# Performance work log

Measured on AMD Instinct MI355X. Metric: run time of the kernel, lower is better.

## Reference

```python
import jax, jax.numpy as jnp
import numpy as np

B, S, DIM = 64, 256, 512
H = 16
DH = DIM // H          # 32
W = 256                # window_size == seq_len
ROPE_BASE = 10000.0


def _rope(x):
    # x: (B, S, H, DH), interleaved-pair RoPE
    pos = jnp.arange(S, dtype=jnp.float32)
    inv_freq = 1.0 / (ROPE_BASE ** (jnp.arange(0, DH, 2, dtype=jnp.float32) / DH))
    sinusoid = pos[:, None] * inv_freq[None, :]            # (S, DH/2)
    sin = jnp.sin(sinusoid)[None, :, None, :]              # (1, S, 1, DH/2)
    cos = jnp.cos(sinusoid)[None, :, None, :]
    x1 = x[..., 0::2]
    x2 = x[..., 1::2]
    r1 = x1 * cos - x2 * sin
    r2 = x1 * sin + x2 * cos
    return jnp.stack([r1, r2], axis=-1).reshape(x.shape)


def setup_inputs() -> dict:
    key = jax.random.key(0)
    ks = jax.random.split(key, 8)
    s = 1.0 / np.sqrt(DIM)
    return {
        "hidden_states": jax.random.normal(ks[0], (B, S, DIM), jnp.float32),
        "Wq": jax.random.normal(ks[1], (DIM, DIM), jnp.float32) * s,
        "bq": jnp.zeros((DIM,), jnp.float32),
        "Wk": jax.random.normal(ks[2], (DIM, DIM), jnp.float32) * s,
        "bk": jnp.zeros((DIM,), jnp.float32),
        "Wv": jax.random.normal(ks[3], (DIM, DIM), jnp.float32) * s,
        "bv": jnp.zeros((DIM,), jnp.float32),
        "bias_table": jax.random.normal(ks[4], (2 * W - 1, H), jnp.float32) * 0.02,
    }


def reference(hidden_states, Wq, bq, Wk, bk, Wv, bv, bias_table):
    b, s, _ = hidden_states.shape
    q = hidden_states @ Wq + bq
    k = hidden_states @ Wk + bk
    v = hidden_states @ Wv + bv
    # (B, S, H, DH)
    q = _rope(q.reshape(b, s, H, DH))
    k = _rope(k.reshape(b, s, H, DH))
    v = v.reshape(b, s, H, DH)
    # (B, H, S, DH)
    q = q.transpose(0, 2, 1, 3)
    k = k.transpose(0, 2, 1, 3)
    v = v.transpose(0, 2, 1, 3)
    scores = jnp.einsum('bhqd,bhkd->bhqk', q, k) / np.sqrt(DH)
    # relative_position_index[i, j] == (i - j) + W - 1
    rel_idx = jnp.arange(W)[:, None] - jnp.arange(W)[None, :] + (W - 1)
    rel_bias = bias_table[rel_idx]                 # (W, W, H)
    rel_bias = rel_bias.transpose(2, 0, 1)[None]   # (1, H, W, W)
    # NOTE: bias added AFTER softmax, faithful to the original module
    probs = jax.nn.softmax(scores, axis=-1) + rel_bias
    ctx = jnp.einsum('bhqk,bhkd->bhqd', probs, v)
    ctx = ctx.transpose(0, 2, 1, 3).reshape(b, s, DIM)
    return ctx
```

## Files before the change

kernel.cpp:

```cpp
#include <hip/hip_runtime.h>
#include <stdint.h>

typedef __attribute__((ext_vector_type(8))) short bf16x8;
typedef __attribute__((ext_vector_type(4))) float f32x4;
typedef __attribute__((ext_vector_type(4))) unsigned int u32x4;

#define MFMA16(a, b, c) __builtin_amdgcn_mfma_f32_16x16x32_bf16(a, b, c, 0, 0, 0)

__device__ __forceinline__ float bf2f(unsigned short u) {
    union { unsigned int i; float f; } x; x.i = ((unsigned int)u) << 16; return x.f;
}
__device__ __forceinline__ unsigned short f2bf(float f) {
    union { float f; unsigned int i; } x; x.f = f;
    unsigned int u = x.i;
    return (unsigned short)((u + 0x7FFFu + ((u >> 16) & 1u)) >> 16);
}

__global__ __launch_bounds__(256) void k_cvt(const float4* __restrict__ in,
                                             unsigned short* __restrict__ At) {
    __shared__ unsigned short t[16 * 512];
    const int tid = threadIdx.x;
    const int blk = blockIdx.x;
#pragma unroll
    for (int it = 0; it < 8; ++it) {
        int idx = it * 256 + tid;
        int row = idx >> 7, col4 = idx & 127;
        float4 v = in[(size_t)(blk * 16 + row) * 128 + col4];
        ushort4 o;
        o.x = f2bf(v.x); o.y = f2bf(v.y); o.z = f2bf(v.z); o.w = f2bf(v.w);
        int addr = row * 512 + (((col4 >> 1) ^ (row & 7)) << 3) + ((col4 & 1) << 2);
        *(ushort4*)&t[addr] = o;
    }
    __syncthreads();
#pragma unroll
    for (int it = 0; it < 4; ++it) {
        int idx = it * 256 + tid;
        int kb = idx >> 6, l = idx & 63;
        int row = l & 15, l4 = l >> 4;
        int c = (kb * 4 + l4) ^ (row & 7);
        bf16x8 v = *(const bf16x8*)&t[row * 512 + c * 8];
        *(bf16x8*)(At + ((size_t)(blk * 16 + kb) << 9) + l * 8) = v;
    }
}

__global__ __launch_bounds__(256) void k_wt(const float* __restrict__ W0,
                                            const float* __restrict__ W1,
                                            const float* __restrict__ W2,
                                            unsigned short* __restrict__ Wt2) {
    int tile = blockIdx.x * 4 + (threadIdx.x >> 6);
    int l = threadIdx.x & 63;
    int nt = tile >> 4;
    int kb = tile & 15;
    int mat = nt >> 5;
    const float* __restrict__ Wm = (mat == 0) ? W0 : (mat == 1) ? W1 : W2;
    int np = (nt & 31) * 16 + (l & 15);
    int k0 = kb * 32 + (l >> 4) * 8;
    bf16x8 o;
#pragma unroll
    for (int e = 0; e < 8; ++e) o[e] = (short)f2bf(Wm[(size_t)(k0 + e) * 512 + np]);
    *(bf16x8*)(Wt2 + (size_t)tile * 512 + l * 8) = o;
}

__global__ __launch_bounds__(256) void k_sc(float* __restrict__ cs2) {
    int s = threadIdx.x;
    for (int f = 0; f < 16; ++f) {
        float inv = powf(10000.0f, -(float)f / 16.0f);
        float a = (float)s * inv;
        cs2[(s * 16 + f) * 2 + 0] = cosf(a);
        cs2[(s * 16 + f) * 2 + 1] = sinf(a);
    }
}

__global__ __launch_bounds__(256, 3) void k_gemm(
    const unsigned short* __restrict__ At,
    const unsigned short* __restrict__ Bt,
    const float* __restrict__ bq, const float* __restrict__ bk, const float* __restrict__ bv,
    const float* __restrict__ cs2,
    unsigned short* __restrict__ Qo, unsigned short* __restrict__ Ko, unsigned short* __restrict__ Vo) {
    const int tid = threadIdx.x;
    const int wave = tid >> 6, lane = tid & 63;
    const int l15 = lane & 15, l4 = lane >> 4;
    int bid = blockIdx.x;
    int swz = (bid & 7) * 384 + (bid >> 3);
    const int m0 = (swz / 24) * 128;
    const int n0 = (swz % 24) * 64;
    const int wm = (wave >> 1) * 64, wn = (wave & 1) * 32;
    const bool isV = (n0 >= 1024);

    f32x4 zero4 = {0.f, 0.f, 0.f, 0.f};
    f32x4 acc[4][2];
#pragma unroll
    for (int i = 0; i < 4; ++i)
#pragma unroll
        for (int j = 0; j < 2; ++j) acc[i][j] = zero4;

    const unsigned short* gA = At + ((size_t)((m0 + wm) >> 4) << 13) + lane * 8;
    const unsigned short* gB = Bt + ((size_t)((n0 + wn) >> 4) << 13) + lane * 8;

#pragma unroll
    for (int kb = 0; kb < 16; ++kb) {
        bf16x8 af[4], bf[2];
#pragma unroll
        for (int i = 0; i < 4; ++i) af[i] = *(const bf16x8*)(gA + (size_t)i * 8192 + kb * 512);
#pragma unroll
        for (int j = 0; j < 2; ++j) bf[j] = *(const bf16x8*)(gB + (size_t)j * 8192 + kb * 512);
        if (!isV) {
#pragma unroll
            for (int i = 0; i < 4; ++i)
#pragma unroll
                for (int j = 0; j < 2; ++j) acc[i][j] = MFMA16(af[i], bf[j], acc[i][j]);
        } else {
#pragma unroll
            for (int i = 0; i < 4; ++i)
#pragma unroll
                for (int j = 0; j < 2; ++j) acc[i][j] = MFMA16(bf[j], af[i], acc[i][j]);
        }
    }

    if (!isV) {
        const int mat = n0 >> 9;
        unsigned short* __restrict__ dst = (mat == 0) ? Qo : Ko;
        const float* __restrict__ bias = (mat == 0) ? bq : bk;
#pragma unroll
        for (int j = 0; j < 2; ++j) {
            int col = (n0 & 511) + wn + j * 16 + l15;
            float bb = bias[col];
            int h = col >> 5, dh = col & 31, f = dh >> 1;
            float sgn = (col & 1) ? 1.0f : -1.0f;
#pragma unroll
            for (int i = 0; i < 4; ++i) {
#pragma unroll
                for (int r = 0; r < 4; ++r) {
                    int m = m0 + wm + i * 16 + l4 * 4 + r;
                    int b2 = m >> 8, s = m & 255;
                    float t = acc[i][j][r] + bb;
                    float partner = __shfl_xor(t, 1);
                    float2 cn = *(const float2*)(cs2 + (s * 16 + f) * 2);
                    float o = t * cn.x + sgn * partner * cn.y;
                    dst[(size_t)(b2 * 16 + h) * 8192 + s * 32 + dh] = f2bf(o);
                }
            }
        }
    } else {
#pragma unroll
        for (int j = 0; j < 2; ++j) {
#pragma unroll
            for (int r = 0; r < 4; ++r) {
                int n = (n0 & 511) + wn + j * 16 + l4 * 4 + r;
                float bb = bv[n];
                int h = n >> 5, dh = n & 31;
#pragma unroll
                for (int i = 0; i < 4; ++i) {
                    int m = m0 + wm + i * 16 + l15;
                    int b2 = m >> 8, s = m & 255;
                    Vo[(size_t)(b2 * 16 + h) * 8192 + dh * 256 + s] = f2bf(acc[i][j][r] + bb);
                }
            }
        }
    }
}

__global__ __launch_bounds__(256, 3) void k_attn(
    const unsigned short* __restrict__ Qm, const unsigned short* __restrict__ Km,
    const unsigned short* __restrict__ Vm,
    const float* __restrict__ bias_table, float* __restrict__ out) {
    __shared__ unsigned short k_l[256 * 32];
    __shared__ unsigned short vt_l[32 * 256];
    __shared__ float bias_g[512];

    const int tid = threadIdx.x, wave = tid >> 6, lane = tid & 63;
    const int l15 = lane & 15, l4 = lane >> 4;
    int bid = blockIdx.x;
    int swz = (bid & 7) * 128 + (bid >> 3);
    const int h = swz & 15, b = swz >> 4;
    const size_t bh = ((size_t)(b * 16 + h)) * 8192;

    for (int i = tid; i < 511; i += 256) bias_g[i] = bias_table[i * 16 + h];

#pragma unroll
    for (int it = 0; it < 4; ++it) {
        int p = it * 256 + wave * 64 + lane;
        __builtin_amdgcn_global_load_lds(
            (const __attribute__((address_space(1))) unsigned int*)(Km + bh + p * 8),
            (__attribute__((address_space(3))) unsigned int*)(k_l + it * 2048 + wave * 512), 16, 0, 0);
    }
#pragma unroll
    for (int it = 0; it < 4; ++it) {
        int p = it * 256 + wave * 64 + lane;
        int dh = p >> 5, cpos = p & 31;
        int srcc = cpos ^ (dh & 7);
        __builtin_amdgcn_global_load_lds(
            (const __attribute__((address_space(1))) unsigned int*)(Vm + bh + dh * 256 + srcc * 8),
            (__attribute__((address_space(3))) unsigned int*)(vt_l + it * 2048 + wave * 512), 16, 0, 0);
    }
    __syncthreads();

    f32x4 zero4 = {0.f, 0.f, 0.f, 0.f};
    const float SCL2 = 0.17677669529663687f * 1.4426950408889634f;
    const int qrow = 16 * wave + l15;
    const bool hi = (l4 >> 1) != 0;
    const bool odd = (l4 & 1) != 0;

    for (int qb = 0; qb < 4; ++qb) {
        const int q0 = qb * 64;
        bf16x8 qfrag = *(const bf16x8*)(Qm + bh + (size_t)(q0 + qrow) * 32 + l4 * 8);

        f32x4 sc[16];
#pragma unroll
        for (int ct = 0; ct < 16; ++ct) {
            bf16x8 kf = *(const bf16x8*)&k_l[(ct * 16 + l15) * 32 + l4 * 8];
            sc[ct] = MFMA16(kf, qfrag, zero4);
        }

        float sum = 0.f;
#pragma unroll
        for (int ct = 0; ct < 16; ++ct) {
#pragma unroll
            for (int r = 0; r < 4; ++r) {
                float e;
                float x = sc[ct][r] * SCL2;
                asm("v_exp_f32 %0, %1" : "=v"(e) : "v"(x));
                sc[ct][r] = e;
                sum += e;
            }
        }
        sum += __shfl_xor(sum, 16);
        sum += __shfl_xor(sum, 32);
        float inv = 1.0f / sum;

        f32x4 o0 = zero4, o1 = zero4;
#pragma unroll
        for (int m = 0; m < 8; ++m) {
            unsigned int E0, E1, O0, O1;
            {
                int kbase = 32 * m + 4 * l4;
                int jb = q0 + qrow - kbase + 255;
                float p0 = sc[2 * m][0] * inv + bias_g[jb];
                float p1 = sc[2 * m][1] * inv + bias_g[jb - 1];
                float p2 = sc[2 * m][2] * inv + bias_g[jb - 2];
                float p3 = sc[2 * m][3] * inv + bias_g[jb - 3];
                asm("v_cvt_pk_bf16_f32 %0, %1, %2" : "=v"(E0) : "v"(p0), "v"(p1));
                asm("v_cvt_pk_bf16_f32 %0, %1, %2" : "=v"(E1) : "v"(p2), "v"(p3));
                jb -= 16;
                p0 = sc[2 * m + 1][0] * inv + bias_g[jb];
                p1 = sc[2 * m + 1][1] * inv + bias_g[jb - 1];
                p2 = sc[2 * m + 1][2] * inv + bias_g[jb - 2];
                p3 = sc[2 * m + 1][3] * inv + bias_g[jb - 3];
                asm("v_cvt_pk_bf16_f32 %0, %1, %2" : "=v"(O0) : "v"(p0), "v"(p1));
                asm("v_cvt_pk_bf16_f32 %0, %1, %2" : "=v"(O1) : "v"(p2), "v"(p3));
            }
            unsigned int m0_ = hi ? O0 : E0, m1_ = hi ? O1 : E1;
            unsigned int s0 = hi ? E0 : O0, s1 = hi ? E1 : O1;
            unsigned int g0 = __shfl_xor(s0, 32), g1 = __shfl_xor(s1, 32);
            unsigned int X00 = hi ? g0 : m0_, X01 = hi ? g1 : m1_;
            unsigned int X10 = hi ? m0_ : g0, X11 = hi ? m1_ : g1;
            unsigned int k0 = odd ? X10 : X00, k1 = odd ? X11 : X01;
            unsigned int t0 = odd ? X00 : X10, t1 = odd ? X01 : X11;
            unsigned int r0 = __shfl_xor(t0, 16), r1 = __shfl_xor(t1, 16);
            union { unsigned int u[4]; bf16x8 v; } pu;
            pu.u[0] = odd ? r0 : k0; pu.u[1] = odd ? r1 : k1;
            pu.u[2] = odd ? k0 : r0; pu.u[3] = odd ? k1 : r1;
            int vc = (m * 4 + l4) ^ (l15 & 7);
            bf16x8 v0 = *(const bf16x8*)&vt_l[l15 * 256 + vc * 8];
            bf16x8 v1 = *(const bf16x8*)&vt_l[(16 + l15) * 256 + vc * 8];
            o0 = MFMA16(pu.v, v0, o0);
            o1 = MFMA16(pu.v, v1, o1);
        }

#pragma unroll
        for (int r = 0; r < 4; ++r) {
            int s = q0 + 16 * wave + l4 * 4 + r;
            float* po = out + ((size_t)(b * 256 + s)) * 512 + h * 32;
            po[l15] = o0[r];
            po[16 + l15] = o1[r];
        }
    }
}

extern "C" void kernel_launch(void* const* d_in, const int* in_sizes, int n_in,
                              void* d_out, int out_size, void* d_ws, size_t ws_size,
                              hipStream_t stream) {
    const float* hs = (const float*)d_in[0];
    const float* Wq = (const float*)d_in[1];
    const float* bq = (const float*)d_in[2];
    const float* Wk = (const float*)d_in[3];
    const float* bk = (const float*)d_in[4];
    const float* Wv = (const float*)d_in[5];
    const float* bv = (const float*)d_in[6];
    const float* bt = (const float*)d_in[7];
    float* out = (float*)d_out;

    char* ws = (char*)d_ws;
    unsigned short* hsb = (unsigned short*)ws;
    unsigned short* wt = (unsigned short*)(ws + 16777216);
    unsigned short* Qo = (unsigned short*)(ws + 18350080);
    unsigned short* Ko = (unsigned short*)(ws + 35127296);
    unsigned short* Vo = (unsigned short*)(ws + 51904512);
    float* cs2 = (float*)(ws + 68681728);

    hipLaunchKernelGGL(k_cvt, dim3(1024), dim3(256), 0, stream, (const float4*)hs, hsb);
    hipLaunchKernelGGL(k_wt, dim3(384), dim3(256), 0, stream, Wq, Wk, Wv, wt);
    hipLaunchKernelGGL(k_sc, dim3(1), dim3(256), 0, stream, cs2);
    hipLaunchKernelGGL(k_gemm, dim3(3072), dim3(256), 0, stream,
                       hsb, wt, bq, bk, bv, cs2, Qo, Ko, Vo);
    hipLaunchKernelGGL(k_attn, dim3(1024), dim3(256), 0, stream,
                       Qo, Ko, Vo, bt, out);
}
```

Measured before the change: 108.0 us.

## Enlarge QKV GEMM tile to 128x128 with double-buffered LDS staging of A

The projection GEMM tile grows from 128x64 to 128x128 per block, halving the grid. The shared A tile is staged into double-buffered LDS with global_load_lds so the four waves share it, while each wave's B fragments come straight from global memory; this cuts redundant global A traffic. The attention kernel also hoists all four Q fragment loads ahead of the initial barrier so they overlap the K/V LDS fills. The trade-off is more accumulator registers and LDS per block (launch bounds still ask for 3 blocks/CU) plus a full barrier every k-step.

After: 173.6 us. 1.61x slower.

```diff
diff --git a/kernel.cpp b/kernel.cpp
--- a/kernel.cpp
+++ b/kernel.cpp
@@ -77,52 +77,94 @@
     const float* __restrict__ bq, const float* __restrict__ bk, const float* __restrict__ bv,
     const float* __restrict__ cs2,
     unsigned short* __restrict__ Qo, unsigned short* __restrict__ Ko, unsigned short* __restrict__ Vo) {
+    __shared__ unsigned short a_l[2][8192];
     const int tid = threadIdx.x;
     const int wave = tid >> 6, lane = tid & 63;
     const int l15 = lane & 15, l4 = lane >> 4;
     int bid = blockIdx.x;
-    int swz = (bid & 7) * 384 + (bid >> 3);
-    const int m0 = (swz / 24) * 128;
-    const int n0 = (swz % 24) * 64;
-    const int wm = (wave >> 1) * 64, wn = (wave & 1) * 32;
+    int swz = (bid & 7) * 192 + (bid >> 3);
+    const int m0 = (swz / 12) * 128;
+    const int n0 = (swz % 12) * 128;
+    const int wm = (wave >> 1) * 64, wn = (wave & 1) * 64;
     const bool isV = (n0 >= 1024);
 
     f32x4 zero4 = {0.f, 0.f, 0.f, 0.f};
-    f32x4 acc[4][2];
+    f32x4 acc[4][4];
 #pragma unroll
     for (int i = 0; i < 4; ++i)
 #pragma unroll
-        for (int j = 0; j < 2; ++j) acc[i][j] = zero4;
-
-    const unsigned short* gA = At + ((size_t)((m0 + wm) >> 4) << 13) + lane * 8;
-    const unsigned short* gB = Bt + ((size_t)((n0 + wn) >> 4) << 13) + lane * 8;
-
-#pragma unroll
-    for (int kb = 0; kb < 16; ++kb) {
-        bf16x8 af[4], bf[2];
-#pragma unroll
-        for (int i = 0; i < 4; ++i) af[i] = *(const bf16x8*)(gA + (size_t)i * 8192 + kb * 512);
-#pragma unroll
-        for (int j = 0; j < 2; ++j) bf[j] = *(const bf16x8*)(gB + (size_t)j * 8192 + kb * 512);
-        if (!isV) {
-#pragma unroll
-            for (int i = 0; i < 4; ++i)
-#pragma unroll
-                for (int j = 0; j < 2; ++j) acc[i][j] = MFMA16(af[i], bf[j], acc[i][j]);
-        } else {
-#pragma unroll
-            for (int i = 0; i < 4; ++i)
-#pragma unroll
-                for (int j = 0; j < 2; ++j) acc[i][j] = MFMA16(bf[j], af[i], acc[i][j]);
-        }
-    }
+        for (int j = 0; j < 4; ++j) acc[i][j] = zero4;
+
+    const unsigned short* gA = At + (((size_t)(m0 >> 4)) << 13) + lane * 8;
+    const unsigned short* gB = Bt + (((size_t)((n0 + wn) >> 4)) << 13) + lane * 8;
+
+#define STAGE(buf, kt)                                                                          \
+    {                                                                                           \
+        _Pragma("unroll")                                                                       \
+        for (int c = 0; c < 4; ++c) {                                                           \
+            int ti = wave * 4 + c;                                                              \
+            int mi = ti >> 1, kbi = ti & 1;                                                     \
+            __builtin_amdgcn_global_load_lds(                                                   \
+                (const __attribute__((address_space(1))) unsigned int*)                         \
+                    (gA + ((size_t)mi << 13) + ((kt) * 2 + kbi) * 512),                         \
+                (__attribute__((address_space(3))) unsigned int*)(&a_l[(buf)][ti * 512]),       \
+                16, 0, 0);                                                                      \
+        }                                                                                       \
+    }
+#define LOADB(breg, kt)                                                                         \
+    {                                                                                           \
+        _Pragma("unroll")                                                                       \
+        for (int kc = 0; kc < 2; ++kc)                                                          \
+            _Pragma("unroll")                                                                   \
+            for (int j = 0; j < 4; ++j)                                                         \
+                breg[kc][j] = *(const bf16x8*)(gB + (size_t)j * 8192 + ((kt) * 2 + kc) * 512);  \
+    }
+#define COMPUTE(buf, breg)                                                                      \
+    {                                                                                           \
+        _Pragma("unroll")                                                                       \
+        for (int kc = 0; kc < 2; ++kc) {                                                        \
+            bf16x8 af[4];                                                                       \
+            _Pragma("unroll")                                                                   \
+            for (int i = 0; i < 4; ++i)                                                         \
+                af[i] = *(const bf16x8*)&a_l[(buf)][((((wave >> 1) * 4 + i) << 1) + kc) * 512 + lane * 8]; \
+            if (!isV) {                                                                         \
+                _Pragma("unroll")                                                               \
+                for (int i = 0; i < 4; ++i)                                                     \
+                    _Pragma("unroll")                                                           \
+                    for (int j = 0; j < 4; ++j)                                                 \
+                        acc[i][j] = MFMA16(af[i], breg[kc][j], acc[i][j]);                      \
+            } else {                                                                            \
+                _Pragma("unroll")                                                               \
+                for (int i = 0; i < 4; ++i)                                                     \
+                    _Pragma("unroll")                                                           \
+                    for (int j = 0; j < 4; ++j)                                                 \
+                        acc[i][j] = MFMA16(breg[kc][j], af[i], acc[i][j]);                      \
+            }                                                                                   \
+        }                                                                                       \
+    }
+#define SYNC() { asm volatile("s_waitcnt vmcnt(0) lgkmcnt(0)" ::: "memory");                    \
+                 __builtin_amdgcn_s_barrier(); }
+
+    bf16x8 b[2][4];
+    STAGE(0, 0);
+    for (int kt = 0; kt < 8; ++kt) {
+        SYNC();
+        const int cur = kt & 1;
+        LOADB(b, kt);
+        if (kt < 7) STAGE(cur ^ 1, kt + 1);
+        COMPUTE(cur, b);
+    }
+#undef STAGE
+#undef LOADB
+#undef COMPUTE
+#undef SYNC
 
     if (!isV) {
         const int mat = n0 >> 9;
         unsigned short* __restrict__ dst = (mat == 0) ? Qo : Ko;
         const float* __restrict__ bias = (mat == 0) ? bq : bk;
 #pragma unroll
-        for (int j = 0; j < 2; ++j) {
+        for (int j = 0; j < 4; ++j) {
             int col = (n0 & 511) + wn + j * 16 + l15;
             float bb = bias[col];
             int h = col >> 5, dh = col & 31, f = dh >> 1;
@@ -143,7 +185,7 @@
         }
     } else {
 #pragma unroll
-        for (int j = 0; j < 2; ++j) {
+        for (int j = 0; j < 4; ++j) {
 #pragma unroll
             for (int r = 0; r < 4; ++r) {
                 int n = (n0 & 511) + wn + j * 16 + l4 * 4 + r;
@@ -193,17 +235,23 @@
             (const __attribute__((address_space(1))) unsigned int*)(Vm + bh + dh * 256 + srcc * 8),
             (__attribute__((address_space(3))) unsigned int*)(vt_l + it * 2048 + wave * 512), 16, 0, 0);
     }
+
+    const int qrow = 16 * wave + l15;
+    bf16x8 qf[4];
+#pragma unroll
+    for (int qb = 0; qb < 4; ++qb)
+        qf[qb] = *(const bf16x8*)(Qm + bh + (size_t)(qb * 64 + qrow) * 32 + l4 * 8);
     __syncthreads();
 
     f32x4 zero4 = {0.f, 0.f, 0.f, 0.f};
     const float SCL2 = 0.17677669529663687f * 1.4426950408889634f;
-    const int qrow = 16 * wave + l15;
     const bool hi = (l4 >> 1) != 0;
     const bool odd = (l4 & 1) != 0;
 
+#pragma unroll 1
     for (int qb = 0; qb < 4; ++qb) {
         const int q0 = qb * 64;
-        bf16x8 qfrag = *(const bf16x8*)(Qm + bh + (size_t)(q0 + qrow) * 32 + l4 * 8);
+        bf16x8 qfrag = qf[qb];
 
         f32x4 sc[16];
 #pragma unroll
@@ -301,7 +349,7 @@
     hipLaunchKernelGGL(k_cvt, dim3(1024), dim3(256), 0, stream, (const float4*)hs, hsb);
     hipLaunchKernelGGL(k_wt, dim3(384), dim3(256), 0, stream, Wq, Wk, Wv, wt);
     hipLaunchKernelGGL(k_sc, dim3(1), dim3(256), 0, stream, cs2);
-    hipLaunchKernelGGL(k_gemm, dim3(3072), dim3(256), 0, stream,
+    hipLaunchKernelGGL(k_gemm, dim3(1536), dim3(256), 0, stream,
                        hsb, wt, bq, bk, bv, cs2, Qo, Ko, Vo);
     hipLaunchKernelGGL(k_attn, dim3(1024), dim3(256), 0, stream,
                        Qo, Ko, Vo, bt, out);
```
